# Optimization experiments

Measured on AMD Instinct MI355X. Metric: run time of the kernel, lower is better.

The kernel has to match this reference:

```python
import jax, jax.numpy as jnp
import numpy as np

N = 50000
E_RAND = 800000
IN_CH = 128
HID = 64
HEADS = 4
OUT_CH = 3
NEG_SLOPE = 0.2
BN_EPS = 1e-5


def setup_inputs() -> dict:
    key = jax.random.key(0)
    ks = jax.random.split(key, 24)
    x = jax.random.normal(ks[0], (N, IN_CH), dtype=jnp.float32)
    er = jax.random.randint(ks[1], (2, E_RAND), 0, N)
    sl = jnp.tile(jnp.arange(N, dtype=er.dtype)[None, :], (2, 1))
    edge_index = jnp.concatenate([er, sl], axis=1)  # [2, 850000]
    s = 0.1
    d1 = HID * HEADS            # 256
    d2 = (HID // 2) * HEADS     # 128
    inp = dict(x=x, edge_index=edge_index)
    # layer 1: in 128 -> heads*64
    inp["W1"] = s * jax.random.normal(ks[2], (IN_CH, HEADS * HID), dtype=jnp.float32)
    inp["a1s"] = s * jax.random.normal(ks[3], (HEADS, HID), dtype=jnp.float32)
    inp["a1d"] = s * jax.random.normal(ks[4], (HEADS, HID), dtype=jnp.float32)
    inp["b1"] = jnp.zeros((d1,), jnp.float32)
    inp["g1"] = jnp.ones((d1,), jnp.float32)
    inp["be1"] = jnp.zeros((d1,), jnp.float32)
    inp["m1"] = 0.01 * jax.random.normal(ks[5], (d1,), dtype=jnp.float32)
    inp["v1"] = jnp.ones((d1,), jnp.float32) + 0.01 * jax.random.uniform(ks[6], (d1,))
    # layer 2: in 256 -> heads*32
    inp["W2"] = s * jax.random.normal(ks[7], (d1, HEADS * (HID // 2)), dtype=jnp.float32)
    inp["a2s"] = s * jax.random.normal(ks[8], (HEADS, HID // 2), dtype=jnp.float32)
    inp["a2d"] = s * jax.random.normal(ks[9], (HEADS, HID // 2), dtype=jnp.float32)
    inp["b2"] = jnp.zeros((d2,), jnp.float32)
    inp["g2"] = jnp.ones((d2,), jnp.float32)
    inp["be2"] = jnp.zeros((d2,), jnp.float32)
    inp["m2"] = 0.01 * jax.random.normal(ks[10], (d2,), dtype=jnp.float32)
    inp["v2"] = jnp.ones((d2,), jnp.float32) + 0.01 * jax.random.uniform(ks[11], (d2,))
    # layer 3: in 128 -> 1 head, out_ch, concat=False
    inp["W3"] = s * jax.random.normal(ks[12], (d2, OUT_CH), dtype=jnp.float32)
    inp["a3s"] = s * jax.random.normal(ks[13], (1, OUT_CH), dtype=jnp.float32)
    inp["a3d"] = s * jax.random.normal(ks[14], (1, OUT_CH), dtype=jnp.float32)
    inp["b3"] = jnp.zeros((OUT_CH,), jnp.float32)
    return inp


def gat_conv(x, src, dst, W, a_src, a_dst, b, heads, fdim, concat):
    n = x.shape[0]
    h = (x @ W).reshape(n, heads, fdim)           # [N,H,F]
    als = jnp.einsum('nhf,hf->nh', h, a_src)      # [N,H]
    ald = jnp.einsum('nhf,hf->nh', h, a_dst)
    e = jax.nn.leaky_relu(als[src] + ald[dst], NEG_SLOPE)  # [E,H]
    m = jax.lax.stop_gradient(jax.ops.segment_max(e, dst, num_segments=n))
    ex = jnp.exp(e - m[dst])
    ssum = jax.ops.segment_sum(ex, dst, num_segments=n)
    alpha = ex / (ssum[dst] + 1e-16)              # segment softmax over in-edges
    msg = h[src] * alpha[:, :, None]              # [E,H,F]
    out = jax.ops.segment_sum(msg, dst, num_segments=n)  # [N,H,F]
    out = out.reshape(n, heads * fdim) if concat else out.mean(axis=1)
    return out + b


def batch_norm(x, gamma, beta, mean, var):
    return (x - mean) * jax.lax.rsqrt(var + BN_EPS) * gamma + beta


def reference(x, edge_index, W1, a1s, a1d, b1, g1, be1, m1, v1,
              W2, a2s, a2d, b2, g2, be2, m2, v2,
              W3, a3s, a3d, b3):
    src, dst = edge_index[0], edge_index[1]
    h = gat_conv(x, src, dst, W1, a1s, a1d, b1, HEADS, HID, True)
    h = jax.nn.elu(batch_norm(h, g1, be1, m1, v1))
    h = gat_conv(h, src, dst, W2, a2s, a2d, b2, HEADS, HID // 2, True)
    h = jax.nn.elu(batch_norm(h, g2, be2, m2, v2))
    h = gat_conv(h, src, dst, W3, a3s, a3d, b3, 1, OUT_CH, False)
    return jax.nn.log_softmax(h, axis=1)
```

## Files before the change

### kernel.cpp

```cpp
#include <hip/hip_runtime.h>


#define WSZ 64

typedef short short8 __attribute__((ext_vector_type(8)));
typedef short short4v __attribute__((ext_vector_type(4)));
typedef float float4v __attribute__((ext_vector_type(4)));

__device__ inline unsigned short f2bf(float f) {
  unsigned u = __float_as_uint(f);
  u += 0x7FFFu + ((u >> 16) & 1u);
  return (unsigned short)(u >> 16);
}
__device__ inline float bf2f(unsigned short u) {
  return __uint_as_float(((unsigned)u) << 16);
}


__global__ __launch_bounds__(256) void hist_kernel(const int* __restrict__ dst, int E,
                                                   int* __restrict__ deg) {
  int e = blockIdx.x * 256 + threadIdx.x;
  if (e < E) atomicAdd(&deg[dst[e]], 1);
}

__global__ __launch_bounds__(256) void block_sums_kernel(const int* __restrict__ deg, int n,
                                                         int* __restrict__ bsum) {
  __shared__ int sh[256];
  int t = threadIdx.x;
  int base = blockIdx.x * 1024 + t * 4;
  int v = 0;
#pragma unroll
  for (int j = 0; j < 4; ++j) {
    int idx = base + j;
    if (idx < n) v += deg[idx];
  }
  sh[t] = v;
  __syncthreads();
  for (int off = 128; off >= 1; off >>= 1) {
    if (t < off) sh[t] += sh[t + off];
    __syncthreads();
  }
  if (t == 0) bsum[blockIdx.x] = sh[0];
}

__global__ void tiny_scan_kernel(int* bsum, int nb) {
  if (threadIdx.x == 0 && blockIdx.x == 0) {
    int run = 0;
    for (int i = 0; i < nb; ++i) {
      int v = bsum[i];
      bsum[i] = run;
      run += v;
    }
  }
}

__global__ __launch_bounds__(256) void scan_write_kernel(const int* __restrict__ deg, int n,
                                                         const int* __restrict__ bbase,
                                                         int* __restrict__ row_start,
                                                         int* __restrict__ cursor) {
  __shared__ int sh[256];
  int t = threadIdx.x;
  int base = blockIdx.x * 1024 + t * 4;
  int v[4];
  int s = 0;
#pragma unroll
  for (int j = 0; j < 4; ++j) {
    int idx = base + j;
    v[j] = (idx < n) ? deg[idx] : 0;
    s += v[j];
  }
  sh[t] = s;
  __syncthreads();
  for (int off = 1; off < 256; off <<= 1) {
    int x = (t >= off) ? sh[t - off] : 0;
    __syncthreads();
    sh[t] += x;
    __syncthreads();
  }
  int excl = sh[t] - s + bbase[blockIdx.x];
#pragma unroll
  for (int j = 0; j < 4; ++j) {
    int idx = base + j;
    if (idx < n) {
      row_start[idx] = excl;
      cursor[idx] = excl;
    }
    excl += v[j];
  }
  if (blockIdx.x == gridDim.x - 1 && t == 255) row_start[n] = excl;
}

__global__ __launch_bounds__(256) void scatter_kernel(const int* __restrict__ src,
                                                      const int* __restrict__ dst, int E,
                                                      int* __restrict__ cursor,
                                                      int* __restrict__ csr_src) {
  int e = blockIdx.x * 256 + threadIdx.x;
  if (e < E) {
    int d = dst[e];
    int p = atomicAdd(&cursor[d], 1);
    csr_src[p] = src[e];
  }
}


__global__ __launch_bounds__(256) void conv_w1t_kernel(const float* __restrict__ W1,
                                                       unsigned short* __restrict__ W1t) {
  int idx = blockIdx.x * 256 + threadIdx.x;
  int n = idx >> 7, k = idx & 127;
  W1t[idx] = f2bf(W1[k * 256 + n]);
}

__global__ __launch_bounds__(256) void conv_w2t_kernel(const float* __restrict__ W2,
                                                       unsigned short* __restrict__ W2t) {
  int idx = blockIdx.x * 256 + threadIdx.x;
  int n = idx >> 8, p = idx & 255;
  int kl = (p & ~63) | ((p & 3) << 4) | ((p >> 2) & 15);
  W2t[idx] = f2bf(W2[kl * 128 + n]);
}


template <int K, int BN, bool AF32>
__global__ __launch_bounds__(256) void gemm_mfma(
    const void* __restrict__ Ap,
    const unsigned short* __restrict__ Bt,
    const float* __restrict__ a_s, const float* __restrict__ a_d,
    unsigned short* __restrict__ hout,
    float* __restrict__ als, float* __restrict__ ald,
    int M) {
  constexpr int CF = BN / 64;
  constexpr int PAD = 36;
  __shared__ unsigned short As[64][PAD];
  __shared__ unsigned short Bs[BN][PAD];
  const int t = threadIdx.x;
  const int w = t >> 6;
  const int lane = t & 63;
  const int c16 = lane & 15;
  const int q = lane >> 4;
  const int bm = blockIdx.x * 64;
  const int arow = t >> 2;
  const int akc = (t & 3) * 8;

  float4v acc[4][CF];
#pragma unroll
  for (int rf = 0; rf < 4; ++rf)
#pragma unroll
    for (int cf = 0; cf < CF; ++cf) acc[rf][cf] = float4v{0.f, 0.f, 0.f, 0.f};

  for (int k0 = 0; k0 < K; k0 += 32) {
    {
      int gr = bm + arow;
      if constexpr (AF32) {
        const float* Af = (const float*)Ap + (size_t)gr * K + k0 + akc;
        float4 v0 = make_float4(0.f, 0.f, 0.f, 0.f), v1 = v0;
        if (gr < M) {
          v0 = *(const float4*)Af;
          v1 = *(const float4*)(Af + 4);
        }
        ushort4 u0, u1;
        u0.x = f2bf(v0.x); u0.y = f2bf(v0.y); u0.z = f2bf(v0.z); u0.w = f2bf(v0.w);
        u1.x = f2bf(v1.x); u1.y = f2bf(v1.y); u1.z = f2bf(v1.z); u1.w = f2bf(v1.w);
        *(ushort4*)&As[arow][akc] = u0;
        *(ushort4*)&As[arow][akc + 4] = u1;
      } else {
        uint4 v = make_uint4(0u, 0u, 0u, 0u);
        if (gr < M) v = *(const uint4*)((const unsigned short*)Ap + (size_t)gr * K + k0 + akc);
        *(uint2*)&As[arow][akc] = make_uint2(v.x, v.y);
        *(uint2*)&As[arow][akc + 4] = make_uint2(v.z, v.w);
      }
    }
#pragma unroll
    for (int h = 0; h < BN / 64; ++h) {
      int n = (t >> 2) + h * 64;
      uint4 v = *(const uint4*)(Bt + (size_t)n * K + k0 + akc);
      *(uint2*)&Bs[n][akc] = make_uint2(v.x, v.y);
      *(uint2*)&Bs[n][akc + 4] = make_uint2(v.z, v.w);
    }
    __syncthreads();
    short8 af[4], bfr[CF];
#pragma unroll
    for (int rf = 0; rf < 4; ++rf) {
      short4v lo = *(short4v*)&As[rf * 16 + c16][q * 8];
      short4v hi = *(short4v*)&As[rf * 16 + c16][q * 8 + 4];
      af[rf] = __builtin_shufflevector(lo, hi, 0, 1, 2, 3, 4, 5, 6, 7);
    }
#pragma unroll
    for (int cf = 0; cf < CF; ++cf) {
      int n = w * (CF * 16) + cf * 16 + c16;
      short4v lo = *(short4v*)&Bs[n][q * 8];
      short4v hi = *(short4v*)&Bs[n][q * 8 + 4];
      bfr[cf] = __builtin_shufflevector(lo, hi, 0, 1, 2, 3, 4, 5, 6, 7);
    }
#pragma unroll
    for (int rf = 0; rf < 4; ++rf)
#pragma unroll
      for (int cf = 0; cf < CF; ++cf)
        acc[rf][cf] =
            __builtin_amdgcn_mfma_f32_16x16x32_bf16(af[rf], bfr[cf], acc[rf][cf], 0, 0, 0);
    __syncthreads();
  }

  float sasv[CF], sadv[CF];
#pragma unroll
  for (int cf = 0; cf < CF; ++cf) {
    int L = w * (CF * 16) + cf * 16 + c16;
    sasv[cf] = a_s[L];
    sadv[cf] = a_d[L];
  }
#pragma unroll
  for (int rf = 0; rf < 4; ++rf) {
#pragma unroll
    for (int r = 0; r < 4; ++r) {
      int n = bm + rf * 16 + q * 4 + r;
      float ps = 0.f, pd = 0.f;
      unsigned short us[CF];
#pragma unroll
      for (int cf = 0; cf < CF; ++cf) {
        float v = acc[rf][cf][r];
        us[cf] = f2bf(v);
        ps += v * sasv[cf];
        pd += v * sadv[cf];
      }
#pragma unroll
      for (int off = 1; off <= 8; off <<= 1) {
        ps += __shfl_xor(ps, off, 16);
        pd += __shfl_xor(pd, off, 16);
      }
      if (n < M) {
        if constexpr (CF == 4) {
          ushort4 u;
          u.x = us[0]; u.y = us[1]; u.z = us[2]; u.w = us[3];
          *(ushort4*)(hout + (size_t)n * BN + w * 64 + c16 * 4) = u;
        } else {
          ushort2 u;
          u.x = us[0]; u.y = us[1];
          *(ushort2*)(hout + (size_t)n * BN + w * 32 + c16 * 2) = u;
        }
        if (c16 == 0) {
          als[(size_t)n * 4 + w] = ps;
          ald[(size_t)n * 4 + w] = pd;
        }
      }
    }
  }
}


template <int D, bool FUSEL3>
__global__ __launch_bounds__(256) void gat_aggregate(
    const unsigned short* __restrict__ h_bf, const float* __restrict__ als,
    const float* __restrict__ ald, const int* __restrict__ row_start,
    const int* __restrict__ csr_src, const float* __restrict__ bias,
    const float* __restrict__ gamma, const float* __restrict__ beta,
    const float* __restrict__ bmean, const float* __restrict__ bvar,
    unsigned short* __restrict__ obf,
    const float* __restrict__ W3, const float* __restrict__ a3s,
    const float* __restrict__ a3d, float4* __restrict__ h3p,
    float* __restrict__ ald3,
    int n_nodes) {
  constexpr int VPT = D / WSZ;
  constexpr int H = 4;
  __shared__ float w3s[384];
  __shared__ float sa3[6];
  if constexpr (FUSEL3) {
    for (int i = threadIdx.x; i < 384; i += 256) w3s[i] = W3[i];
    if (threadIdx.x < 3) {
      sa3[threadIdx.x] = a3s[threadIdx.x];
      sa3[3 + threadIdx.x] = a3d[threadIdx.x];
    }
    __syncthreads();
  }
  int wid = threadIdx.x >> 6, lane = threadIdx.x & 63;
  int n = blockIdx.x * 4 + wid;
  if (n >= n_nodes) return;
  int c = lane * VPT;
  int hd = lane >> 4;
  float aldv = ald[(size_t)n * H + hd];
  int row = row_start[n], end = row_start[n + 1];
  float acc[VPT] = {};
  float ssum = 0.f;
  int i = row;

#define EDGE_BLOCK(B)                                                          \
  for (; i + (B) - 1 < end; i += (B)) {                                        \
    int s[B];                                                                  \
    float e[B];                                                                \
    _Pragma("unroll") for (int j = 0; j < (B); ++j) s[j] = csr_src[i + j];     \
    _Pragma("unroll") for (int j = 0; j < (B); ++j) e[j] =                     \
        als[(size_t)s[j] * H + hd] + aldv;                                     \
    if constexpr (VPT == 4) {                                                  \
      ushort4 u[B];                                                            \
      _Pragma("unroll") for (int j = 0; j < (B); ++j) u[j] =                   \
          *(const ushort4*)(h_bf + (size_t)s[j] * D + c);                      \
      _Pragma("unroll") for (int j = 0; j < (B); ++j) {                        \
        float ee = e[j];                                                       \
        ee = (ee > 0.f) ? ee : 0.2f * ee;                                      \
        float ex = __expf(ee);                                                 \
        ssum += ex;                                                            \
        acc[0] += ex * bf2f(u[j].x);                                           \
        acc[1] += ex * bf2f(u[j].y);                                           \
        acc[2] += ex * bf2f(u[j].z);                                           \
        acc[3] += ex * bf2f(u[j].w);                                           \
      }                                                                        \
    } else {                                                                   \
      ushort2 u[B];                                                            \
      _Pragma("unroll") for (int j = 0; j < (B); ++j) u[j] =                   \
          *(const ushort2*)(h_bf + (size_t)s[j] * D + c);                      \
      _Pragma("unroll") for (int j = 0; j < (B); ++j) {                        \
        float ee = e[j];                                                       \
        ee = (ee > 0.f) ? ee : 0.2f * ee;                                      \
        float ex = __expf(ee);                                                 \
        ssum += ex;                                                            \
        acc[0] += ex * bf2f(u[j].x);                                           \
        acc[1] += ex * bf2f(u[j].y);                                           \
      }                                                                        \
    }                                                                          \
  }

  EDGE_BLOCK(8)
  EDGE_BLOCK(4)
  EDGE_BLOCK(1)
#undef EDGE_BLOCK

  float inv = 1.f / (ssum + 1e-16f);
#pragma unroll
  for (int j = 0; j < VPT; ++j) {
    int cl = hd * (VPT * 16) + j * 16 + (lane & 15);
    float o = acc[j] * inv + bias[cl];
    o = (o - bmean[cl]) * rsqrtf(bvar[cl] + 1e-5f) * gamma[cl] + beta[cl];
    o = (o > 0.f) ? o : (__expf(o) - 1.f);
    acc[j] = o;
  }
  if constexpr (!FUSEL3) {
    ushort4 u;
    u.x = f2bf(acc[0]); u.y = f2bf(acc[1]); u.z = f2bf(acc[2]); u.w = f2bf(acc[3]);
    *(ushort4*)(obf + (size_t)n * D + c) = u;
  } else {
    int k0l = hd * 32 + (lane & 15);
    int k1l = k0l + 16;
    float p0 = acc[0] * w3s[k0l * 3 + 0] + acc[1] * w3s[k1l * 3 + 0];
    float p1 = acc[0] * w3s[k0l * 3 + 1] + acc[1] * w3s[k1l * 3 + 1];
    float p2 = acc[0] * w3s[k0l * 3 + 2] + acc[1] * w3s[k1l * 3 + 2];
#pragma unroll
    for (int off = 32; off >= 1; off >>= 1) {
      p0 += __shfl_xor(p0, off, 64);
      p1 += __shfl_xor(p1, off, 64);
      p2 += __shfl_xor(p2, off, 64);
    }
    if (lane == 0) {
      float als3 = p0 * sa3[0] + p1 * sa3[1] + p2 * sa3[2];
      float ad3 = p0 * sa3[3] + p1 * sa3[4] + p2 * sa3[5];
      h3p[n] = make_float4(p0, p1, p2, als3);
      ald3[n] = ad3;
    }
  }
}


__global__ __launch_bounds__(256) void l3_agg_kernel(const float4* __restrict__ h3p,
                                                     const float* __restrict__ ald3,
                                                     const int* __restrict__ row_start,
                                                     const int* __restrict__ csr_src,
                                                     const float* __restrict__ b3,
                                                     float* __restrict__ out, int n_nodes) {
  int wid = threadIdx.x >> 6, lane = threadIdx.x & 63;
  int n = blockIdx.x * 4 + wid;
  if (n >= n_nodes) return;
  float aldv = ald3[n];
  int row = row_start[n], end = row_start[n + 1];
  float a0 = 0.f, a1 = 0.f, a2 = 0.f, ss = 0.f;
  for (int i = row + lane; i < end; i += 64) {
    int s = csr_src[i];
    float4 hv = h3p[s];
    float e = hv.w + aldv;
    e = (e > 0.f) ? e : 0.2f * e;
    float ex = __expf(e);
    ss += ex;
    a0 += ex * hv.x;
    a1 += ex * hv.y;
    a2 += ex * hv.z;
  }
#pragma unroll
  for (int off = 32; off >= 1; off >>= 1) {
    a0 += __shfl_xor(a0, off, 64);
    a1 += __shfl_xor(a1, off, 64);
    a2 += __shfl_xor(a2, off, 64);
    ss += __shfl_xor(ss, off, 64);
  }
  if (lane == 0) {
    float inv = 1.f / (ss + 1e-16f);
    float o0 = a0 * inv + b3[0];
    float o1 = a1 * inv + b3[1];
    float o2 = a2 * inv + b3[2];
    float m = fmaxf(o0, fmaxf(o1, o2));
    float lse = m + logf(expf(o0 - m) + expf(o1 - m) + expf(o2 - m));
    out[n * 3 + 0] = o0 - lse;
    out[n * 3 + 1] = o1 - lse;
    out[n * 3 + 2] = o2 - lse;
  }
}


extern "C" void kernel_launch(void* const* d_in, const int* in_sizes, int n_in,
                              void* d_out, int out_size, void* d_ws, size_t ws_size,
                              hipStream_t stream) {
  const float* x   = (const float*)d_in[0];
  const int*   ei  = (const int*)d_in[1];
  const float* W1  = (const float*)d_in[2];
  const float* a1s = (const float*)d_in[3];
  const float* a1d = (const float*)d_in[4];
  const float* b1  = (const float*)d_in[5];
  const float* g1v = (const float*)d_in[6];
  const float* be1 = (const float*)d_in[7];
  const float* m1  = (const float*)d_in[8];
  const float* v1  = (const float*)d_in[9];
  const float* W2  = (const float*)d_in[10];
  const float* a2s = (const float*)d_in[11];
  const float* a2d = (const float*)d_in[12];
  const float* b2  = (const float*)d_in[13];
  const float* g2v = (const float*)d_in[14];
  const float* be2 = (const float*)d_in[15];
  const float* m2  = (const float*)d_in[16];
  const float* v2  = (const float*)d_in[17];
  const float* W3  = (const float*)d_in[18];
  const float* a3s = (const float*)d_in[19];
  const float* a3d = (const float*)d_in[20];
  const float* b3  = (const float*)d_in[21];
  float* out = (float*)d_out;

  const int N = in_sizes[0] / 128;
  const int E = in_sizes[1] / 2;
  const int* srcv = ei;
  const int* dstv = ei + E;

  float* wsf  = (float*)d_ws;
  float* als1 = wsf;
  float* ald1 = als1 + (size_t)N * 4;
  float* als2 = ald1 + (size_t)N * 4;
  float* ald2 = als2 + (size_t)N * 4;
  float* h3p  = ald2 + (size_t)N * 4;
  float* ald3 = h3p + (size_t)N * 4;
  unsigned short* h_bf1 = (unsigned short*)(ald3 + N);
  unsigned short* o1_bf = h_bf1 + (size_t)N * 256;
  unsigned short* h_bf2 = o1_bf + (size_t)N * 256;
  unsigned short* W1t   = h_bf2 + (size_t)N * 128;
  unsigned short* W2t   = W1t + 256 * 128;
  int* deg       = (int*)(W2t + 128 * 256);
  int* row_start = deg + N;
  int* cursor    = row_start + (N + 1);
  int* csr_src   = cursor + (N + 1);
  int* bsum      = csr_src + E;

  const int eb = (E + 255) / 256;
  const int nb = (N + 1023) / 1024;
  const int nodes4 = (N + 3) / 4;
  const int mblocks = (N + 63) / 64;

  conv_w1t_kernel<<<128, 256, 0, stream>>>(W1, W1t);
  conv_w2t_kernel<<<128, 256, 0, stream>>>(W2, W2t);

  hipMemsetAsync(deg, 0, (size_t)N * sizeof(int), stream);
  hist_kernel<<<eb, 256, 0, stream>>>(dstv, E, deg);
  block_sums_kernel<<<nb, 256, 0, stream>>>(deg, N, bsum);
  tiny_scan_kernel<<<1, 64, 0, stream>>>(bsum, nb);
  scan_write_kernel<<<nb, 256, 0, stream>>>(deg, N, bsum, row_start, cursor);
  scatter_kernel<<<eb, 256, 0, stream>>>(srcv, dstv, E, cursor, csr_src);

  gemm_mfma<128, 256, true><<<mblocks, 256, 0, stream>>>(x, W1t, a1s, a1d, h_bf1, als1,
                                                         ald1, N);
  gat_aggregate<256, false><<<nodes4, 256, 0, stream>>>(
      h_bf1, als1, ald1, row_start, csr_src, b1, g1v, be1, m1, v1, o1_bf, nullptr, nullptr,
      nullptr, nullptr, nullptr, N);
  gemm_mfma<256, 128, false><<<mblocks, 256, 0, stream>>>(o1_bf, W2t, a2s, a2d, h_bf2, als2,
                                                          ald2, N);
  gat_aggregate<128, true><<<nodes4, 256, 0, stream>>>(
      h_bf2, als2, ald2, row_start, csr_src, b2, g2v, be2, m2, v2, nullptr, W3, a3s, a3d,
      (float4*)h3p, ald3, N);
  l3_agg_kernel<<<nodes4, 256, 0, stream>>>((const float4*)h3p, ald3, row_start, csr_src,
                                            b3, out, N);
}
```

Measured before the change: 382.4 us.

## Restructure GEMM to keep B in LDS and stream A fragments from global

Replaces the tiled GEMM with a version that loads the whole K extent of a half-width B slice into shared memory once, splits the output columns across a second grid dimension (two heads per block), and has each wave read its A fragments straight from global memory with a one-step register prefetch. This removes the per-K-step syncthreads and the A staging through LDS. The fp32 input x is now converted to bf16 by a separate pre-pass kernel. The aggregate kernel also unpacks bf16 pairs with 32-bit loads and shift/mask operations. The trade-offs are an extra conversion kernel, A being read twice across the column grid, and uncoalesced per-lane A loads.

```diff
diff --git a/kernel.cpp b/kernel.cpp
--- a/kernel.cpp
+++ b/kernel.cpp
@@ -4,16 +4,12 @@
 #define WSZ 64
 
 typedef short short8 __attribute__((ext_vector_type(8)));
-typedef short short4v __attribute__((ext_vector_type(4)));
 typedef float float4v __attribute__((ext_vector_type(4)));
 
 __device__ inline unsigned short f2bf(float f) {
   unsigned u = __float_as_uint(f);
   u += 0x7FFFu + ((u >> 16) & 1u);
   return (unsigned short)(u >> 16);
-}
-__device__ inline float bf2f(unsigned short u) {
-  return __uint_as_float(((unsigned)u) << 16);
 }
 
 
@@ -103,6 +99,17 @@
 }
 
 
+__global__ __launch_bounds__(256) void conv_bf16x4(const float* __restrict__ in,
+                                                   unsigned short* __restrict__ out, int n4) {
+  int i = blockIdx.x * 256 + threadIdx.x;
+  if (i < n4) {
+    float4 v = ((const float4*)in)[i];
+    ushort4 u;
+    u.x = f2bf(v.x); u.y = f2bf(v.y); u.z = f2bf(v.z); u.w = f2bf(v.w);
+    ((ushort4*)out)[i] = u;
+  }
+}
+
 __global__ __launch_bounds__(256) void conv_w1t_kernel(const float* __restrict__ W1,
                                                        unsigned short* __restrict__ W1t) {
   int idx = blockIdx.x * 256 + threadIdx.x;
@@ -119,125 +126,126 @@
 }
 
 
-template <int K, int BN, bool AF32>
-__global__ __launch_bounds__(256) void gemm_mfma(
-    const void* __restrict__ Ap,
+template <int K, int NTOT>
+__global__ __launch_bounds__(256) void gemm_mfma2(
+    const unsigned short* __restrict__ A,
     const unsigned short* __restrict__ Bt,
     const float* __restrict__ a_s, const float* __restrict__ a_d,
     unsigned short* __restrict__ hout,
     float* __restrict__ als, float* __restrict__ ald,
     int M) {
-  constexpr int CF = BN / 64;
-  constexpr int PAD = 36;
-  __shared__ unsigned short As[64][PAD];
-  __shared__ unsigned short Bs[BN][PAD];
+  constexpr int COLS = NTOT / 2;
+  constexpr int CFW = COLS / 16;
+  constexpr int HLOG = NTOT / 4;
+  constexpr int CFH = HLOG / 16;
+  constexpr int VPT = NTOT / 64;
+  constexpr int KS = K / 32;
+  __shared__ __align__(16) unsigned short Bs[COLS][K + 8];
+
   const int t = threadIdx.x;
   const int w = t >> 6;
   const int lane = t & 63;
   const int c16 = lane & 15;
   const int q = lane >> 4;
-  const int bm = blockIdx.x * 64;
-  const int arow = t >> 2;
-  const int akc = (t & 3) * 8;
-
-  float4v acc[4][CF];
-#pragma unroll
-  for (int rf = 0; rf < 4; ++rf)
-#pragma unroll
-    for (int cf = 0; cf < CF; ++cf) acc[rf][cf] = float4v{0.f, 0.f, 0.f, 0.f};
-
-  for (int k0 = 0; k0 < K; k0 += 32) {
-    {
-      int gr = bm + arow;
-      if constexpr (AF32) {
-        const float* Af = (const float*)Ap + (size_t)gr * K + k0 + akc;
-        float4 v0 = make_float4(0.f, 0.f, 0.f, 0.f), v1 = v0;
-        if (gr < M) {
-          v0 = *(const float4*)Af;
-          v1 = *(const float4*)(Af + 4);
-        }
-        ushort4 u0, u1;
-        u0.x = f2bf(v0.x); u0.y = f2bf(v0.y); u0.z = f2bf(v0.z); u0.w = f2bf(v0.w);
-        u1.x = f2bf(v1.x); u1.y = f2bf(v1.y); u1.z = f2bf(v1.z); u1.w = f2bf(v1.w);
-        *(ushort4*)&As[arow][akc] = u0;
-        *(ushort4*)&As[arow][akc + 4] = u1;
-      } else {
-        uint4 v = make_uint4(0u, 0u, 0u, 0u);
-        if (gr < M) v = *(const uint4*)((const unsigned short*)Ap + (size_t)gr * K + k0 + akc);
-        *(uint2*)&As[arow][akc] = make_uint2(v.x, v.y);
-        *(uint2*)&As[arow][akc + 4] = make_uint2(v.z, v.w);
-      }
-    }
-#pragma unroll
-    for (int h = 0; h < BN / 64; ++h) {
-      int n = (t >> 2) + h * 64;
-      uint4 v = *(const uint4*)(Bt + (size_t)n * K + k0 + akc);
-      *(uint2*)&Bs[n][akc] = make_uint2(v.x, v.y);
-      *(uint2*)&Bs[n][akc + 4] = make_uint2(v.z, v.w);
-    }
-    __syncthreads();
-    short8 af[4], bfr[CF];
-#pragma unroll
-    for (int rf = 0; rf < 4; ++rf) {
-      short4v lo = *(short4v*)&As[rf * 16 + c16][q * 8];
-      short4v hi = *(short4v*)&As[rf * 16 + c16][q * 8 + 4];
-      af[rf] = __builtin_shufflevector(lo, hi, 0, 1, 2, 3, 4, 5, 6, 7);
-    }
-#pragma unroll
-    for (int cf = 0; cf < CF; ++cf) {
-      int n = w * (CF * 16) + cf * 16 + c16;
-      short4v lo = *(short4v*)&Bs[n][q * 8];
-      short4v hi = *(short4v*)&Bs[n][q * 8 + 4];
-      bfr[cf] = __builtin_shufflevector(lo, hi, 0, 1, 2, 3, 4, 5, 6, 7);
-    }
-#pragma unroll
-    for (int rf = 0; rf < 4; ++rf)
-#pragma unroll
-      for (int cf = 0; cf < CF; ++cf)
+  const int gcol = blockIdx.y;
+  const int bm = blockIdx.x * 128;
+
+  {
+    constexpr int TPR = K / 64;
+    int nloc = t / TPR;
+    int part = (t % TPR) * 64;
+    const unsigned short* srcp = Bt + (size_t)(gcol * COLS + nloc) * K + part;
+#pragma unroll
+    for (int j = 0; j < 8; ++j) {
+      uint4 v = *(const uint4*)(srcp + j * 8);
+      *(uint4*)&Bs[nloc][part + j * 8] = v;
+    }
+  }
+  int arow[2];
+  arow[0] = min(bm + w * 32 + c16, M - 1);
+  arow[1] = min(bm + w * 32 + 16 + c16, M - 1);
+  short8 afr[2];
+#pragma unroll
+  for (int rf = 0; rf < 2; ++rf)
+    afr[rf] = *(const short8*)(A + (size_t)arow[rf] * K + q * 8);
+  __syncthreads();
+
+  float4v acc[2][CFW];
+#pragma unroll
+  for (int rf = 0; rf < 2; ++rf)
+#pragma unroll
+    for (int cf = 0; cf < CFW; ++cf) acc[rf][cf] = float4v{0.f, 0.f, 0.f, 0.f};
+
+#pragma unroll
+  for (int ks = 0; ks < KS; ++ks) {
+    short8 anx[2];
+    if (ks + 1 < KS) {
+#pragma unroll
+      for (int rf = 0; rf < 2; ++rf)
+        anx[rf] = *(const short8*)(A + (size_t)arow[rf] * K + (ks + 1) * 32 + q * 8);
+    }
+#pragma unroll
+    for (int cf = 0; cf < CFW; ++cf) {
+      short8 bfrag = *(const short8*)&Bs[cf * 16 + c16][ks * 32 + q * 8];
+#pragma unroll
+      for (int rf = 0; rf < 2; ++rf)
         acc[rf][cf] =
-            __builtin_amdgcn_mfma_f32_16x16x32_bf16(af[rf], bfr[cf], acc[rf][cf], 0, 0, 0);
-    __syncthreads();
-  }
-
-  float sasv[CF], sadv[CF];
-#pragma unroll
-  for (int cf = 0; cf < CF; ++cf) {
-    int L = w * (CF * 16) + cf * 16 + c16;
+            __builtin_amdgcn_mfma_f32_16x16x32_bf16(afr[rf], bfrag, acc[rf][cf], 0, 0, 0);
+    }
+    if (ks + 1 < KS) {
+      afr[0] = anx[0];
+      afr[1] = anx[1];
+    }
+  }
+
+  float sasv[CFW], sadv[CFW];
+#pragma unroll
+  for (int cf = 0; cf < CFW; ++cf) {
+    int L = gcol * COLS + cf * 16 + c16;
     sasv[cf] = a_s[L];
     sadv[cf] = a_d[L];
   }
 #pragma unroll
-  for (int rf = 0; rf < 4; ++rf) {
+  for (int rf = 0; rf < 2; ++rf) {
 #pragma unroll
     for (int r = 0; r < 4; ++r) {
-      int n = bm + rf * 16 + q * 4 + r;
-      float ps = 0.f, pd = 0.f;
-      unsigned short us[CF];
-#pragma unroll
-      for (int cf = 0; cf < CF; ++cf) {
+      int n = bm + w * 32 + rf * 16 + q * 4 + r;
+      float ps[2] = {0.f, 0.f}, pd[2] = {0.f, 0.f};
+      unsigned short us[CFW];
+#pragma unroll
+      for (int cf = 0; cf < CFW; ++cf) {
         float v = acc[rf][cf][r];
         us[cf] = f2bf(v);
-        ps += v * sasv[cf];
-        pd += v * sadv[cf];
+        ps[cf / CFH] += v * sasv[cf];
+        pd[cf / CFH] += v * sadv[cf];
       }
 #pragma unroll
       for (int off = 1; off <= 8; off <<= 1) {
-        ps += __shfl_xor(ps, off, 16);
-        pd += __shfl_xor(pd, off, 16);
+#pragma unroll
+        for (int hl = 0; hl < 2; ++hl) {
+          ps[hl] += __shfl_xor(ps[hl], off, 16);
+          pd[hl] += __shfl_xor(pd[hl], off, 16);
+        }
       }
       if (n < M) {
-        if constexpr (CF == 4) {
-          ushort4 u;
-          u.x = us[0]; u.y = us[1]; u.z = us[2]; u.w = us[3];
-          *(ushort4*)(hout + (size_t)n * BN + w * 64 + c16 * 4) = u;
-        } else {
-          ushort2 u;
-          u.x = us[0]; u.y = us[1];
-          *(ushort2*)(hout + (size_t)n * BN + w * 32 + c16 * 2) = u;
-        }
-        if (c16 == 0) {
-          als[(size_t)n * 4 + w] = ps;
-          ald[(size_t)n * 4 + w] = pd;
+#pragma unroll
+        for (int hl = 0; hl < 2; ++hl) {
+          int head = gcol * 2 + hl;
+          unsigned short* dst = hout + (size_t)n * NTOT + head * HLOG + c16 * VPT;
+          if constexpr (VPT == 4) {
+            ushort4 u;
+            u.x = us[hl * 4 + 0]; u.y = us[hl * 4 + 1];
+            u.z = us[hl * 4 + 2]; u.w = us[hl * 4 + 3];
+            *(ushort4*)dst = u;
+          } else {
+            ushort2 u;
+            u.x = us[hl * 2 + 0]; u.y = us[hl * 2 + 1];
+            *(ushort2*)dst = u;
+          }
+          if (c16 == 0) {
+            als[(size_t)n * 4 + head] = ps[hl];
+            ald[(size_t)n * 4 + head] = pd[hl];
+          }
         }
       }
     }
@@ -288,30 +296,30 @@
     _Pragma("unroll") for (int j = 0; j < (B); ++j) e[j] =                     \
         als[(size_t)s[j] * H + hd] + aldv;                                     \
     if constexpr (VPT == 4) {                                                  \
-      ushort4 u[B];                                                            \
+      uint2 u[B];                                                              \
       _Pragma("unroll") for (int j = 0; j < (B); ++j) u[j] =                   \
-          *(const ushort4*)(h_bf + (size_t)s[j] * D + c);                      \
+          *(const uint2*)(h_bf + (size_t)s[j] * D + c);                        \
       _Pragma("unroll") for (int j = 0; j < (B); ++j) {                        \
         float ee = e[j];                                                       \
         ee = (ee > 0.f) ? ee : 0.2f * ee;                                      \
         float ex = __expf(ee);                                                 \
         ssum += ex;                                                            \
-        acc[0] += ex * bf2f(u[j].x);                                           \
-        acc[1] += ex * bf2f(u[j].y);                                           \
-        acc[2] += ex * bf2f(u[j].z);                                           \
-        acc[3] += ex * bf2f(u[j].w);                                           \
+        acc[0] += ex * __uint_as_float(u[j].x << 16);                          \
+        acc[1] += ex * __uint_as_float(u[j].x & 0xFFFF0000u);                  \
+        acc[2] += ex * __uint_as_float(u[j].y << 16);                          \
+        acc[3] += ex * __uint_as_float(u[j].y & 0xFFFF0000u);                  \
       }                                                                        \
     } else {                                                                   \
-      ushort2 u[B];                                                            \
+      unsigned u[B];                                                           \
       _Pragma("unroll") for (int j = 0; j < (B); ++j) u[j] =                   \
-          *(const ushort2*)(h_bf + (size_t)s[j] * D + c);                      \
+          *(const unsigned*)(h_bf + (size_t)s[j] * D + c);                     \
       _Pragma("unroll") for (int j = 0; j < (B); ++j) {                        \
         float ee = e[j];                                                       \
         ee = (ee > 0.f) ? ee : 0.2f * ee;                                      \
         float ex = __expf(ee);                                                 \
         ssum += ex;                                                            \
-        acc[0] += ex * bf2f(u[j].x);                                           \
-        acc[1] += ex * bf2f(u[j].y);                                           \
+        acc[0] += ex * __uint_as_float(u[j] << 16);                            \
+        acc[1] += ex * __uint_as_float(u[j] & 0xFFFF0000u);                    \
       }                                                                        \
     }                                                                          \
   }
@@ -439,7 +447,8 @@
   float* ald2 = als2 + (size_t)N * 4;
   float* h3p  = ald2 + (size_t)N * 4;
   float* ald3 = h3p + (size_t)N * 4;
-  unsigned short* h_bf1 = (unsigned short*)(ald3 + N);
+  unsigned short* x_bf  = (unsigned short*)(ald3 + N);
+  unsigned short* h_bf1 = x_bf + (size_t)N * 128;
   unsigned short* o1_bf = h_bf1 + (size_t)N * 256;
   unsigned short* h_bf2 = o1_bf + (size_t)N * 256;
   unsigned short* W1t   = h_bf2 + (size_t)N * 128;
@@ -453,8 +462,9 @@
   const int eb = (E + 255) / 256;
   const int nb = (N + 1023) / 1024;
   const int nodes4 = (N + 3) / 4;
-  const int mblocks = (N + 63) / 64;
-
+  const dim3 gemm_grid((N + 127) / 128, 2);
+
+  conv_bf16x4<<<(N * 128 / 4 + 255) / 256, 256, 0, stream>>>(x, x_bf, N * 128 / 4);
   conv_w1t_kernel<<<128, 256, 0, stream>>>(W1, W1t);
   conv_w2t_kernel<<<128, 256, 0, stream>>>(W2, W2t);
 
@@ -465,13 +475,13 @@
   scan_write_kernel<<<nb, 256, 0, stream>>>(deg, N, bsum, row_start, cursor);
   scatter_kernel<<<eb, 256, 0, stream>>>(srcv, dstv, E, cursor, csr_src);
 
-  gemm_mfma<128, 256, true><<<mblocks, 256, 0, stream>>>(x, W1t, a1s, a1d, h_bf1, als1,
-                                                         ald1, N);
+  gemm_mfma2<128, 256><<<gemm_grid, 256, 0, stream>>>(x_bf, W1t, a1s, a1d, h_bf1, als1,
+                                                      ald1, N);
   gat_aggregate<256, false><<<nodes4, 256, 0, stream>>>(
       h_bf1, als1, ald1, row_start, csr_src, b1, g1v, be1, m1, v1, o1_bf, nullptr, nullptr,
       nullptr, nullptr, nullptr, N);
-  gemm_mfma<256, 128, false><<<mblocks, 256, 0, stream>>>(o1_bf, W2t, a2s, a2d, h_bf2, als2,
-                                                          ald2, N);
+  gemm_mfma2<256, 128><<<gemm_grid, 256, 0, stream>>>(o1_bf, W2t, a2s, a2d, h_bf2, als2,
+                                                      ald2, N);
   gat_aggregate<128, true><<<nodes4, 256, 0, stream>>>(
       h_bf2, als2, ald2, row_start, csr_src, b2, g2v, be2, m2, v2, nullptr, W3, a3s, a3d,
       (float4*)h3p, ald3, N);
```

Result: no change. 388.8 us (+1.6%).
